# Optimization experiments

Measured on AMD Instinct MI355X. Metric: run time of the kernel, lower is better.

The kernel has to match this reference:

```python
import jax, jax.numpy as jnp
import numpy as np

INPUT, HIDDEN, OUT = 784, 64, 10
N_TEST = 10000
WVEC = INPUT * HIDDEN + HIDDEN + HIDDEN * OUT + OUT  # 50890
B = 64


def setup_inputs() -> dict:
    key = jax.random.key(0)
    k1, k2, k3, k4, k5 = jax.random.split(key, 5)
    inp1 = jax.random.normal(k1, (B, WVEC), dtype=jnp.float32)
    tar1 = jax.random.normal(k2, (B, WVEC), dtype=jnp.float32)
    inp2 = jax.random.normal(k3, (B, WVEC), dtype=jnp.float32)
    tar2 = jax.random.randint(k4, (B, N_TEST), 0, OUT, dtype=jnp.int64)
    images = jax.random.uniform(k5, (N_TEST, INPUT), dtype=jnp.float32)
    return {"inp1": inp1, "tar1": tar1, "inp2": inp2, "tar2": tar2, "images": images}


def _split_weights(w):
    # w: [B, 50890] -> W1 [B,H,I], B1 [B,H], W2 [B,O,H], B2 [B,O]
    b = w.shape[0]
    o1 = INPUT * HIDDEN
    o2 = o1 + HIDDEN
    o3 = o2 + HIDDEN * OUT
    W1 = w[:, :o1].reshape(b, HIDDEN, INPUT)
    B1 = w[:, o1:o2]
    W2 = w[:, o2:o3].reshape(b, OUT, HIDDEN)
    B2 = w[:, o3:]
    return W1, B1, W2, B2


def reference(inp1, tar1, inp2, tar2, images):
    # loss1: MSE * 20
    loss1 = 20.0 * jnp.mean(jnp.square(inp1 - tar1))
    # loss2: per-sample weight-conditioned MLP over fixed dataset, cross entropy
    W1, B1, W2, B2 = _split_weights(inp2)
    h = jax.nn.relu(jnp.einsum('nd,bhd->bnh', images, W1) + B1[:, None, :])   # [B,N,H]
    logits = jnp.einsum('bnh,boh->bno', h, W2) + B2[:, None, :]               # [B,N,O]
    logp = jax.nn.log_softmax(logits, axis=-1)
    ce = -jnp.take_along_axis(logp, tar2[..., None], axis=-1).squeeze(-1)     # [B,N]
    loss2 = jnp.mean(ce)  # mean over images per sample, then mean over batch
    combined = loss1 + loss2
    return (combined, loss1, loss2)
```

## Files before the change

### kernel.cpp

```cpp
#include <hip/hip_runtime.h>
#include <hip/hip_bf16.h>
#include <stdint.h>

#define INPUT_D 784
#define HIDDEN  64
#define OUTC    10
#define NTEST   10000
#define WVEC    50890
#define NBATCH  64
#define O1      50176
#define O2      50240
#define O3      50880
#define KPAD8   896
#define MPAD    10240
#define MTILES  80
#define NCOLS   4096
#define KTILES  7
#define H2      136
#define SCALE1  0x7F7F7F7Fu
#define CAST_ROWS (MPAD + NCOLS)
#define CAST_GROUPS (CAST_ROWS * (KPAD8/4))

typedef __attribute__((ext_vector_type(8))) short  short8;
typedef __attribute__((ext_vector_type(4))) float  floatx4;
typedef __attribute__((ext_vector_type(4))) int    int4v;
typedef __attribute__((ext_vector_type(8))) int    int8v;

__device__ inline void async_copy16(const void* g, void* lds) {
  __builtin_amdgcn_global_load_lds(
      (const __attribute__((address_space(1))) void*)g,
      (__attribute__((address_space(3))) void*)lds, 16, 0, 0);
}

__global__ void prep_kernel(const float* __restrict__ img, const float* __restrict__ inp2,
                            const float* __restrict__ l1a, const float* __restrict__ l1b,
                            uint8_t* __restrict__ outI, uint8_t* __restrict__ outW,
                            float* __restrict__ accum) {
  const int gtid = blockIdx.x * blockDim.x + threadIdx.x;
  const int nthr = gridDim.x * blockDim.x;
  for (int i = gtid; i < CAST_GROUPS; i += nthr) {
    const int row = i / 224;
    const int c   = (i - row * 224) * 4;
    const float* src;
    uint8_t* dst;
    bool valid;
    if (row < MPAD) {
      valid = (row < NTEST);
      src = img + (size_t)row * INPUT_D;
      dst = outI + (size_t)row * KPAD8;
    } else {
      const int rr = row - MPAD;
      valid = true;
      src = inp2 + (size_t)(rr >> 6) * WVEC + (rr & 63) * INPUT_D;
      dst = outW + (size_t)rr * KPAD8;
    }
    float4 v = make_float4(0.f, 0.f, 0.f, 0.f);
    if (valid && (c + 4) <= INPUT_D) v = *(const float4*)(src + c);
    uint32_t w = 0;
    w = __builtin_amdgcn_cvt_pk_fp8_f32(v.x, v.y, w, false);
    w = __builtin_amdgcn_cvt_pk_fp8_f32(v.z, v.w, w, true);
    *(uint32_t*)(dst + c) = w;
  }
  const int n4 = (NBATCH * WVEC) / 4;
  const float4* A4 = (const float4*)l1a;
  const float4* B4 = (const float4*)l1b;
  float s = 0.f;
  for (int i = gtid; i < n4; i += nthr) {
    float4 x = A4[i], y = B4[i];
    float d0 = x.x - y.x, d1 = x.y - y.y, d2 = x.z - y.z, d3 = x.w - y.w;
    s += d0 * d0 + d1 * d1 + d2 * d2 + d3 * d3;
  }
  for (int off = 32; off; off >>= 1) s += __shfl_down(s, off);
  __shared__ float r[4];
  if ((threadIdx.x & 63) == 0) r[threadIdx.x >> 6] = s;
  __syncthreads();
  if (threadIdx.x == 0) atomicAdd(accum, r[0] + r[1] + r[2] + r[3]);
}

__global__ __launch_bounds__(256)
void gemm_fused(const uint8_t* __restrict__ A,
                const uint8_t* __restrict__ Bm,
                const float* __restrict__ inp2,
                const int* __restrict__ tar2,
                float* __restrict__ accums) {
  __shared__ __align__(16) char smem[65536];
  uint8_t* Abuf[2] = {(uint8_t*)smem,           (uint8_t*)(smem + 32768)};
  uint8_t* Bbuf[2] = {(uint8_t*)(smem + 16384), (uint8_t*)(smem + 49152)};
  __hip_bfloat16* hlds  = (__hip_bfloat16*)smem;
  __hip_bfloat16* w2lds = (__hip_bfloat16*)(smem + 34816);
  float*          B2s   = (float*)(smem + 38912);
  int*            tars  = (int*)(smem + 38992);
  float*          red   = (float*)(smem + 40016);

  const int tid  = threadIdx.x;
  const int lane = tid & 63;
  const int wave = tid >> 6;
  const int wr   = (wave >> 1) * 64;
  const int wc   = (wave & 1) * 64;
  const int row0 = blockIdx.x * 128;
  const int col0 = blockIdx.y * 128;
  const int bbase = col0 >> 6;

  floatx4 acc[4][4];
#pragma unroll
  for (int i = 0; i < 4; ++i)
#pragma unroll
    for (int j = 0; j < 4; ++j) acc[i][j] = (floatx4){0.f, 0.f, 0.f, 0.f};

  const int lr   = lane >> 3;
  const int lcB  = (((lane & 7) ^ lr) * 16);
  const int sxor = lane & 7;
  const int q    = lane >> 4;
  const int c0   = (2 * q) ^ sxor;
  const int c1   = c0 ^ 1;

  const uint8_t* Ag = A  + (size_t)(row0 + wave * 32 + lr) * KPAD8 + lcB;
  const uint8_t* Bg = Bm + (size_t)(col0 + wave * 32 + lr) * KPAD8 + lcB;

#pragma unroll
  for (int c = 0; c < 4; ++c) {
    async_copy16(Ag + (size_t)(c * 8) * KPAD8, Abuf[0] + (wave * 4 + c) * 1024);
    async_copy16(Bg + (size_t)(c * 8) * KPAD8, Bbuf[0] + (wave * 4 + c) * 1024);
  }

#pragma unroll
  for (int kt = 0; kt < KTILES; ++kt) {
    __syncthreads();
    if (kt + 1 < KTILES) {
      const int k0 = (kt + 1) * 128;
#pragma unroll
      for (int c = 0; c < 4; ++c) {
        async_copy16(Ag + (size_t)(c * 8) * KPAD8 + k0, Abuf[(kt + 1) & 1] + (wave * 4 + c) * 1024);
        async_copy16(Bg + (size_t)(c * 8) * KPAD8 + k0, Bbuf[(kt + 1) & 1] + (wave * 4 + c) * 1024);
      }
    }
    const uint8_t* Asrc = Abuf[kt & 1];
    const uint8_t* Bsrc = Bbuf[kt & 1];
    int8v b8[4];
#pragma unroll
    for (int ni = 0; ni < 4; ++ni) {
      const uint8_t* base = Bsrc + (wc + ni * 16 + (lane & 15)) * 128;
      int4v lo = *(const int4v*)(base + c0 * 16);
      int4v hi = *(const int4v*)(base + c1 * 16);
      b8[ni] = (int8v){lo.x, lo.y, lo.z, lo.w, hi.x, hi.y, hi.z, hi.w};
    }
#pragma unroll
    for (int mi = 0; mi < 4; ++mi) {
      const uint8_t* base = Asrc + (wr + mi * 16 + (lane & 15)) * 128;
      int4v lo = *(const int4v*)(base + c0 * 16);
      int4v hi = *(const int4v*)(base + c1 * 16);
      int8v a8 = (int8v){lo.x, lo.y, lo.z, lo.w, hi.x, hi.y, hi.z, hi.w};
#pragma unroll
      for (int ni = 0; ni < 4; ++ni)
        acc[mi][ni] = __builtin_amdgcn_mfma_scale_f32_16x16x128_f8f6f4(
            a8, b8[ni], acc[mi][ni], 0 , 0 ,
            0, SCALE1, 0, SCALE1);
    }
  }
  __syncthreads();

  for (int i = tid; i < 2048; i += 256) {
    const int bi = i >> 10, rem = i & 1023;
    const int o = rem >> 6, k = rem & 63;
    float v = (o < OUTC) ? inp2[(size_t)(bbase + bi) * WVEC + O2 + o * HIDDEN + k] : 0.f;
    w2lds[i] = __float2bfloat16(v);
  }
  if (tid < 20) B2s[tid] = inp2[(size_t)(bbase + tid / 10) * WVEC + O3 + tid % 10];
  {
    const int bi = tid >> 7, m = tid & 127;
    const int sample = row0 + m;
    tars[tid] = (sample < NTEST) ? tar2[(size_t)(bbase + bi) * NTEST + sample] : 0;
  }
#pragma unroll
  for (int ni = 0; ni < 4; ++ni) {
    const int n = wc + ni * 16 + (lane & 15);
    const float b1 = inp2[(size_t)(bbase + (n >> 6)) * WVEC + O1 + (n & 63)];
#pragma unroll
    for (int mi = 0; mi < 4; ++mi) {
      const int m = wr + mi * 16 + q * 4;
#pragma unroll
      for (int r = 0; r < 4; ++r) {
        float v = acc[mi][ni][r] + b1;
        hlds[(size_t)(m + r) * H2 + n] = __float2bfloat16(v > 0.f ? v : 0.f);
      }
    }
  }
  __syncthreads();

  const int col = lane & 15;
  float celocal = 0.f;
#pragma unroll
  for (int i = 0; i < 4; ++i) {
    const int task = wave * 4 + i;
    const int mt = task & 7;
    const int bi = task >> 3;
    short8 af0 = *(const short8*)&hlds[(size_t)(mt * 16 + col) * H2 + bi * 64 + q * 8];
    short8 af1 = *(const short8*)&hlds[(size_t)(mt * 16 + col) * H2 + bi * 64 + 32 + q * 8];
    short8 bf0 = *(const short8*)&w2lds[(bi * 16 + col) * 64 + q * 8];
    short8 bf1 = *(const short8*)&w2lds[(bi * 16 + col) * 64 + 32 + q * 8];
    floatx4 lacc = (floatx4){0.f, 0.f, 0.f, 0.f};
    lacc = __builtin_amdgcn_mfma_f32_16x16x32_bf16(af0, bf0, lacc, 0, 0, 0);
    lacc = __builtin_amdgcn_mfma_f32_16x16x32_bf16(af1, bf1, lacc, 0, 0, 0);
    const float b2 = (col < OUTC) ? B2s[bi * OUTC + col] : 0.f;
#pragma unroll
    for (int r = 0; r < 4; ++r) {
      float lv = (col < OUTC) ? (lacc[r] + b2) : -1e30f;
      float mx = lv;
      mx = fmaxf(mx, __shfl_xor(mx, 1));
      mx = fmaxf(mx, __shfl_xor(mx, 2));
      mx = fmaxf(mx, __shfl_xor(mx, 4));
      mx = fmaxf(mx, __shfl_xor(mx, 8));
      float ex = __expf(lv - mx);
      float sm = ex;
      sm += __shfl_xor(sm, 1);
      sm += __shfl_xor(sm, 2);
      sm += __shfl_xor(sm, 4);
      sm += __shfl_xor(sm, 8);
      const float lse = mx + __logf(sm);
      const int row = mt * 16 + q * 4 + r;
      const int tar = tars[bi * 128 + row];
      if (col == tar && (row0 + row) < NTEST) celocal += (lse - lv);
    }
  }
  for (int off = 32; off; off >>= 1) celocal += __shfl_down(celocal, off);
  if (lane == 0) red[wave] = celocal;
  __syncthreads();
  if (tid == 0) atomicAdd(&accums[1], red[0] + red[1] + red[2] + red[3]);
}

__global__ void finalize(const float* __restrict__ accums, float* __restrict__ out) {
  const float l1 = 20.f * accums[0] / (float)(NBATCH * WVEC);
  const float l2 = accums[1] / (float)(NBATCH * NTEST);
  out[0] = l1 + l2;
  out[1] = l1;
  out[2] = l2;
}

__global__ void loss1_fb(const float* __restrict__ a, const float* __restrict__ b,
                         float* __restrict__ accum) {
  const int n4 = (NBATCH * WVEC) / 4;
  const float4* A4 = (const float4*)a;
  const float4* B4 = (const float4*)b;
  float s = 0.f;
  for (int i = blockIdx.x * blockDim.x + threadIdx.x; i < n4; i += gridDim.x * blockDim.x) {
    float4 x = A4[i], y = B4[i];
    float d0 = x.x - y.x, d1 = x.y - y.y, d2 = x.z - y.z, d3 = x.w - y.w;
    s += d0 * d0 + d1 * d1 + d2 * d2 + d3 * d3;
  }
  for (int off = 32; off; off >>= 1) s += __shfl_down(s, off);
  __shared__ float r[4];
  if ((threadIdx.x & 63) == 0) r[threadIdx.x >> 6] = s;
  __syncthreads();
  if (threadIdx.x == 0) atomicAdd(accum, r[0] + r[1] + r[2] + r[3]);
}

__global__ void naive_ce(const float* __restrict__ inp2, const int* __restrict__ tar2,
                         const float* __restrict__ images, float* __restrict__ accum) {
  const int id = blockIdx.x * blockDim.x + threadIdx.x;
  float ce = 0.f;
  if (id < NBATCH * NTEST) {
    const int b = id / NTEST, n = id % NTEST;
    const float* w = inp2 + (size_t)b * WVEC;
    const float* im = images + (size_t)n * INPUT_D;
    float h[HIDDEN];
    for (int hh = 0; hh < HIDDEN; ++hh) {
      float s = w[O1 + hh];
      for (int d = 0; d < INPUT_D; ++d) s = fmaf(im[d], w[hh * INPUT_D + d], s);
      h[hh] = s > 0.f ? s : 0.f;
    }
    float mx = -1e30f, lg[OUTC];
    for (int o = 0; o < OUTC; ++o) {
      float s = w[O3 + o];
      for (int hh = 0; hh < HIDDEN; ++hh) s = fmaf(h[hh], w[O2 + o * HIDDEN + hh], s);
      lg[o] = s;
      mx = fmaxf(mx, s);
    }
    float sm = 0.f;
    for (int o = 0; o < OUTC; ++o) sm += __expf(lg[o] - mx);
    const float lse = mx + __logf(sm);
    const int t = tar2[(size_t)b * NTEST + n];
    float lt = lg[0];
    for (int o = 1; o < OUTC; ++o) lt = (o == t) ? lg[o] : lt;
    ce = lse - lt;
  }
  for (int off = 32; off; off >>= 1) ce += __shfl_down(ce, off);
  __shared__ float r[4];
  if ((threadIdx.x & 63) == 0) r[threadIdx.x >> 6] = ce;
  __syncthreads();
  if (threadIdx.x == 0) atomicAdd(accum, r[0] + r[1] + r[2] + r[3]);
}

extern "C" void kernel_launch(void* const* d_in, const int* in_sizes, int n_in,
                              void* d_out, int out_size, void* d_ws, size_t ws_size,
                              hipStream_t stream) {
  const float* inp1   = (const float*)d_in[0];
  const float* tar1   = (const float*)d_in[1];
  const float* inp2   = (const float*)d_in[2];
  const int*   tar2   = (const int*)d_in[3];
  const float* images = (const float*)d_in[4];
  float*       out    = (float*)d_out;

  const size_t img_bytes  = (size_t)MPAD * KPAD8;
  const size_t wall_bytes = (size_t)NCOLS * KPAD8;
  const size_t needed     = 256 + img_bytes + wall_bytes;

  if (ws_size >= needed) {
    float* accums = (float*)d_ws;
    uint8_t* imgb = (uint8_t*)d_ws + 256;
    uint8_t* wall = (uint8_t*)d_ws + 256 + img_bytes;
    hipMemsetAsync(d_ws, 0, 256, stream);
    prep_kernel<<<1024, 256, 0, stream>>>(images, inp2, inp1, tar1, imgb, wall, accums);
    gemm_fused<<<dim3(MTILES, 32), 256, 0, stream>>>(imgb, wall, inp2, tar2, accums);
    finalize<<<1, 1, 0, stream>>>(accums, out);
  } else {
    hipMemsetAsync(d_out, 0, 3 * sizeof(float), stream);
    loss1_fb<<<1024, 256, 0, stream>>>(inp1, tar1, out + 1);
    naive_ce<<<(NBATCH * NTEST + 255) / 256, 256, 0, stream>>>(inp2, tar2, images, out + 2);
    finalize<<<1, 1, 0, stream>>>(out + 1, out);
  }
}
```

Measured before the change: 194.5 us.

## Move loss1 reduction into GEMM, drop memset/finalize launches, single-buffer LDS

The MSE reduction moves out of the prep kernel into the first k-step of the fused GEMM, where it overlaps the first async tile load. The memset and finalize launches are removed: prep zeroes the accumulators, and the last GEMM block, found with an atomic counter, writes the final losses. The GEMM also drops LDS double buffering for a single buffer with a load-then-sync pattern, lowering LDS use so more blocks can be resident per CU. The cost is that global loads no longer overlap MFMA within a block, and the MSE work now delays the first tile of every GEMM block.

```diff
diff --git a/kernel.cpp b/kernel.cpp
--- a/kernel.cpp
+++ b/kernel.cpp
@@ -14,12 +14,15 @@
 #define KPAD8   896
 #define MPAD    10240
 #define MTILES  80
+#define NBLK    (MTILES * 32)
 #define NCOLS   4096
 #define KTILES  7
 #define H2      136
 #define SCALE1  0x7F7F7F7Fu
 #define CAST_ROWS (MPAD + NCOLS)
 #define CAST_GROUPS (CAST_ROWS * (KPAD8/4))
+#define PREP_BLOCKS 1024
+#define L1N4 ((NBATCH * WVEC) / 4)
 
 typedef __attribute__((ext_vector_type(8))) short  short8;
 typedef __attribute__((ext_vector_type(4))) float  floatx4;
@@ -33,9 +36,13 @@
 }
 
 __global__ void prep_kernel(const float* __restrict__ img, const float* __restrict__ inp2,
-                            const float* __restrict__ l1a, const float* __restrict__ l1b,
                             uint8_t* __restrict__ outI, uint8_t* __restrict__ outW,
-                            float* __restrict__ accum) {
+                            float* __restrict__ accums) {
+  if (blockIdx.x == 0 && threadIdx.x == 0) {
+    *(unsigned int*)&accums[0] = 0u;
+    accums[1] = 0.f;
+    accums[2] = 0.f;
+  }
   const int gtid = blockIdx.x * blockDim.x + threadIdx.x;
   const int nthr = gridDim.x * blockDim.x;
   for (int i = gtid; i < CAST_GROUPS; i += nthr) {
@@ -61,20 +68,6 @@
     w = __builtin_amdgcn_cvt_pk_fp8_f32(v.z, v.w, w, true);
     *(uint32_t*)(dst + c) = w;
   }
-  const int n4 = (NBATCH * WVEC) / 4;
-  const float4* A4 = (const float4*)l1a;
-  const float4* B4 = (const float4*)l1b;
-  float s = 0.f;
-  for (int i = gtid; i < n4; i += nthr) {
-    float4 x = A4[i], y = B4[i];
-    float d0 = x.x - y.x, d1 = x.y - y.y, d2 = x.z - y.z, d3 = x.w - y.w;
-    s += d0 * d0 + d1 * d1 + d2 * d2 + d3 * d3;
-  }
-  for (int off = 32; off; off >>= 1) s += __shfl_down(s, off);
-  __shared__ float r[4];
-  if ((threadIdx.x & 63) == 0) r[threadIdx.x >> 6] = s;
-  __syncthreads();
-  if (threadIdx.x == 0) atomicAdd(accum, r[0] + r[1] + r[2] + r[3]);
 }
 
 __global__ __launch_bounds__(256)
@@ -82,15 +75,18 @@
                 const uint8_t* __restrict__ Bm,
                 const float* __restrict__ inp2,
                 const int* __restrict__ tar2,
-                float* __restrict__ accums) {
-  __shared__ __align__(16) char smem[65536];
-  uint8_t* Abuf[2] = {(uint8_t*)smem,           (uint8_t*)(smem + 32768)};
-  uint8_t* Bbuf[2] = {(uint8_t*)(smem + 16384), (uint8_t*)(smem + 49152)};
+                const float* __restrict__ l1a, const float* __restrict__ l1b,
+                float* __restrict__ accums,
+                float* __restrict__ out) {
+  __shared__ __align__(16) char smem[40036];
+  uint8_t* Alds = (uint8_t*)smem;
+  uint8_t* Blds = (uint8_t*)(smem + 16384);
   __hip_bfloat16* hlds  = (__hip_bfloat16*)smem;
   __hip_bfloat16* w2lds = (__hip_bfloat16*)(smem + 34816);
   float*          B2s   = (float*)(smem + 38912);
   int*            tars  = (int*)(smem + 38992);
   float*          red   = (float*)(smem + 40016);
+  int*            flag  = (int*)(smem + 40032);
 
   const int tid  = threadIdx.x;
   const int lane = tid & 63;
@@ -117,47 +113,51 @@
   const uint8_t* Ag = A  + (size_t)(row0 + wave * 32 + lr) * KPAD8 + lcB;
   const uint8_t* Bg = Bm + (size_t)(col0 + wave * 32 + lr) * KPAD8 + lcB;
 
-#pragma unroll
-  for (int c = 0; c < 4; ++c) {
-    async_copy16(Ag + (size_t)(c * 8) * KPAD8, Abuf[0] + (wave * 4 + c) * 1024);
-    async_copy16(Bg + (size_t)(c * 8) * KPAD8, Bbuf[0] + (wave * 4 + c) * 1024);
-  }
-
-#pragma unroll
   for (int kt = 0; kt < KTILES; ++kt) {
+    const int k0 = kt * 128;
+#pragma unroll
+    for (int c = 0; c < 4; ++c) {
+      const int ch = wave * 4 + c;
+      async_copy16(Ag + (size_t)(c * 8) * KPAD8 + k0, Alds + ch * 1024);
+      async_copy16(Bg + (size_t)(c * 8) * KPAD8 + k0, Blds + ch * 1024);
+    }
+    if (kt == 0) {
+      const int bid = blockIdx.y * gridDim.x + blockIdx.x;
+      float s = 0.f;
+      for (int i = bid * 256 + tid; i < L1N4; i += NBLK * 256) {
+        float4 x = ((const float4*)l1a)[i];
+        float4 y = ((const float4*)l1b)[i];
+        float d0 = x.x - y.x, d1 = x.y - y.y, d2 = x.z - y.z, d3 = x.w - y.w;
+        s += d0 * d0 + d1 * d1 + d2 * d2 + d3 * d3;
+      }
+      for (int off = 32; off; off >>= 1) s += __shfl_down(s, off);
+      if (lane == 0) atomicAdd(&accums[2], s);
+    }
     __syncthreads();
-    if (kt + 1 < KTILES) {
-      const int k0 = (kt + 1) * 128;
-#pragma unroll
-      for (int c = 0; c < 4; ++c) {
-        async_copy16(Ag + (size_t)(c * 8) * KPAD8 + k0, Abuf[(kt + 1) & 1] + (wave * 4 + c) * 1024);
-        async_copy16(Bg + (size_t)(c * 8) * KPAD8 + k0, Bbuf[(kt + 1) & 1] + (wave * 4 + c) * 1024);
-      }
-    }
-    const uint8_t* Asrc = Abuf[kt & 1];
-    const uint8_t* Bsrc = Bbuf[kt & 1];
-    int8v b8[4];
+    int8v a8[4], b8[4];
 #pragma unroll
     for (int ni = 0; ni < 4; ++ni) {
-      const uint8_t* base = Bsrc + (wc + ni * 16 + (lane & 15)) * 128;
+      const uint8_t* base = Blds + (wc + ni * 16 + (lane & 15)) * 128;
       int4v lo = *(const int4v*)(base + c0 * 16);
       int4v hi = *(const int4v*)(base + c1 * 16);
       b8[ni] = (int8v){lo.x, lo.y, lo.z, lo.w, hi.x, hi.y, hi.z, hi.w};
     }
 #pragma unroll
     for (int mi = 0; mi < 4; ++mi) {
-      const uint8_t* base = Asrc + (wr + mi * 16 + (lane & 15)) * 128;
+      const uint8_t* base = Alds + (wr + mi * 16 + (lane & 15)) * 128;
       int4v lo = *(const int4v*)(base + c0 * 16);
       int4v hi = *(const int4v*)(base + c1 * 16);
-      int8v a8 = (int8v){lo.x, lo.y, lo.z, lo.w, hi.x, hi.y, hi.z, hi.w};
+      a8[mi] = (int8v){lo.x, lo.y, lo.z, lo.w, hi.x, hi.y, hi.z, hi.w};
+    }
+#pragma unroll
+    for (int mi = 0; mi < 4; ++mi)
 #pragma unroll
       for (int ni = 0; ni < 4; ++ni)
         acc[mi][ni] = __builtin_amdgcn_mfma_scale_f32_16x16x128_f8f6f4(
-            a8, b8[ni], acc[mi][ni], 0 , 0 ,
+            a8[mi], b8[ni], acc[mi][ni], 0 , 0 ,
             0, SCALE1, 0, SCALE1);
-    }
-  }
-  __syncthreads();
+    __syncthreads();
+  }
 
   for (int i = tid; i < 2048; i += 256) {
     const int bi = i >> 10, rem = i & 1023;
@@ -225,20 +225,25 @@
   for (int off = 32; off; off >>= 1) celocal += __shfl_down(celocal, off);
   if (lane == 0) red[wave] = celocal;
   __syncthreads();
-  if (tid == 0) atomicAdd(&accums[1], red[0] + red[1] + red[2] + red[3]);
-}
-
-__global__ void finalize(const float* __restrict__ accums, float* __restrict__ out) {
-  const float l1 = 20.f * accums[0] / (float)(NBATCH * WVEC);
-  const float l2 = accums[1] / (float)(NBATCH * NTEST);
-  out[0] = l1 + l2;
-  out[1] = l1;
-  out[2] = l2;
+  if (tid == 0) {
+    atomicAdd(&accums[1], red[0] + red[1] + red[2] + red[3]);
+    __threadfence();
+    unsigned int old = atomicAdd((unsigned int*)&accums[0], 1u);
+    *flag = (old == (unsigned int)(NBLK - 1)) ? 1 : 0;
+  }
+  __syncthreads();
+  if (*flag && tid == 0) {
+    const float l1 = 20.f * atomicAdd(&accums[2], 0.f) / (float)(NBATCH * WVEC);
+    const float l2 = atomicAdd(&accums[1], 0.f) / (float)(NBATCH * NTEST);
+    out[0] = l1 + l2;
+    out[1] = l1;
+    out[2] = l2;
+  }
 }
 
 __global__ void loss1_fb(const float* __restrict__ a, const float* __restrict__ b,
                          float* __restrict__ accum) {
-  const int n4 = (NBATCH * WVEC) / 4;
+  const int n4 = L1N4;
   const float4* A4 = (const float4*)a;
   const float4* B4 = (const float4*)b;
   float s = 0.f;
@@ -290,6 +295,14 @@
   if (threadIdx.x == 0) atomicAdd(accum, r[0] + r[1] + r[2] + r[3]);
 }
 
+__global__ void finalize_fb(const float* __restrict__ accums, float* __restrict__ out) {
+  const float l1 = 20.f * accums[0] / (float)(NBATCH * WVEC);
+  const float l2 = accums[1] / (float)(NBATCH * NTEST);
+  out[0] = l1 + l2;
+  out[1] = l1;
+  out[2] = l2;
+}
+
 extern "C" void kernel_launch(void* const* d_in, const int* in_sizes, int n_in,
                               void* d_out, int out_size, void* d_ws, size_t ws_size,
                               hipStream_t stream) {
@@ -300,22 +313,22 @@
   const float* images = (const float*)d_in[4];
   float*       out    = (float*)d_out;
 
+  const size_t acc_bytes  = 256;
   const size_t img_bytes  = (size_t)MPAD * KPAD8;
   const size_t wall_bytes = (size_t)NCOLS * KPAD8;
-  const size_t needed     = 256 + img_bytes + wall_bytes;
+  const size_t needed     = acc_bytes + img_bytes + wall_bytes;
 
   if (ws_size >= needed) {
     float* accums = (float*)d_ws;
-    uint8_t* imgb = (uint8_t*)d_ws + 256;
-    uint8_t* wall = (uint8_t*)d_ws + 256 + img_bytes;
-    hipMemsetAsync(d_ws, 0, 256, stream);
-    prep_kernel<<<1024, 256, 0, stream>>>(images, inp2, inp1, tar1, imgb, wall, accums);
-    gemm_fused<<<dim3(MTILES, 32), 256, 0, stream>>>(imgb, wall, inp2, tar2, accums);
-    finalize<<<1, 1, 0, stream>>>(accums, out);
+    uint8_t* imgb = (uint8_t*)d_ws + acc_bytes;
+    uint8_t* wall = (uint8_t*)d_ws + acc_bytes + img_bytes;
+    prep_kernel<<<PREP_BLOCKS, 256, 0, stream>>>(images, inp2, imgb, wall, accums);
+    gemm_fused<<<dim3(MTILES, 32), 256, 0, stream>>>(imgb, wall, inp2, tar2,
+                                                     inp1, tar1, accums, out);
   } else {
     hipMemsetAsync(d_out, 0, 3 * sizeof(float), stream);
     loss1_fb<<<1024, 256, 0, stream>>>(inp1, tar1, out + 1);
     naive_ce<<<(NBATCH * NTEST + 255) / 256, 256, 0, stream>>>(inp2, tar2, images, out + 2);
-    finalize<<<1, 1, 0, stream>>>(out + 1, out);
-  }
-}
+    finalize_fb<<<1, 1, 0, stream>>>(out + 1, out);
+  }
+}
```

Result: slower. 318.0 us (+63.5%).
